# Kernel tuning notes

Hardware: AMD Instinct MI355X
Metric: run time of the kernel (lower is better)

Reference implementation:

```python
import jax, jax.numpy as jnp
import numpy as np

EMBED_DIM = 1024
N_HEADS = 16
DK = EMBED_DIM // N_HEADS


def setup_inputs() -> dict:
    key = jax.random.key(0)
    ks = jax.random.split(key, 9)
    s = 1.0 / np.sqrt(EMBED_DIM)
    d = EMBED_DIM
    return {
        "x": jax.random.normal(ks[0], (2, 2048, d), dtype=jnp.float32),
        "Wq": jax.random.uniform(ks[1], (d, d), jnp.float32, -s, s),
        "bq": jax.random.uniform(ks[2], (d,), jnp.float32, -s, s),
        "Wk": jax.random.uniform(ks[3], (d, d), jnp.float32, -s, s),
        "bk": jax.random.uniform(ks[4], (d,), jnp.float32, -s, s),
        "Wv": jax.random.uniform(ks[5], (d, d), jnp.float32, -s, s),
        "bv": jax.random.uniform(ks[6], (d,), jnp.float32, -s, s),
        "Wo": jax.random.uniform(ks[7], (d, d), jnp.float32, -s, s),
        "bo": jax.random.uniform(ks[8], (d,), jnp.float32, -s, s),
    }


def reference(x, Wq, bq, Wk, bk, Wv, bv, Wo, bo):
    B, S, D = x.shape
    H, dk = N_HEADS, DK
    # QKV projections
    q = (x @ Wq + bq).reshape(B, S, H, dk).transpose(0, 2, 1, 3)  # [B,H,S,dk]
    k = (x @ Wk + bk).reshape(B, S, H, dk).transpose(0, 2, 1, 3)
    v = (x @ Wv + bv).reshape(B, S, H, dk).transpose(0, 2, 1, 3)
    # scaled dot-product attention with full score matrix (faithful to source)
    scores = jnp.einsum("bhqd,bhkd->bhqk", q, k) / jnp.sqrt(jnp.float32(dk))
    attn = jax.nn.softmax(scores, axis=-1)
    out = jnp.einsum("bhqk,bhkd->bhqd", attn, v)  # [B,H,S,dk]
    out = out.transpose(0, 2, 1, 3).reshape(B, S, D)
    return out @ Wo + bo
```

## Files before the change

### kernel.cpp

```cpp
#include <hip/hip_runtime.h>

typedef unsigned short u16;
typedef unsigned int u32;
typedef __attribute__((ext_vector_type(8))) short short8;
typedef __attribute__((ext_vector_type(4))) float float4v;

struct alignas(8) U16x4 { u16 x, y, z, w; };

__device__ __forceinline__ u16 f2b(float f) {
    union { float f; unsigned int u; } v; v.f = f;
    unsigned int r = (v.u >> 16) & 1u;
    v.u += 0x7fffu + r;
    return (u16)(v.u >> 16);
}

__device__ __forceinline__ float b2f(u16 u) {
    union { unsigned int u; float f; } v; v.u = ((u32)u) << 16; return v.f;
}

__device__ __forceinline__ void gld16(const u16* g, u16* l) {
    __builtin_amdgcn_global_load_lds(
        (const __attribute__((address_space(1))) void*)g,
        (__attribute__((address_space(3))) void*)l, 16, 0, 0);
}

__device__ __forceinline__ short8 frag8(const u16* base, int row, int cg) {
    return *(const short8*)(base + row * 64 + ((cg ^ (row & 7)) << 3));
}

__global__ __launch_bounds__(256) void prep_kernel(
    const float* __restrict__ x, const float* __restrict__ W0,
    const float* __restrict__ W1, const float* __restrict__ W2,
    const float* __restrict__ W3, u16* __restrict__ xb,
    u16* __restrict__ T0, u16* __restrict__ T1,
    u16* __restrict__ T2, u16* __restrict__ T3) {
    __shared__ float tile[32][33];
    int id = blockIdx.x;
    if (id < 4096) {
        size_t i = ((size_t)id * 256 + threadIdx.x) * 4;
        float4 v = *(const float4*)(x + i);
        U16x4 o;
        o.x = f2b(v.x); o.y = f2b(v.y); o.z = f2b(v.z); o.w = f2b(v.w);
        *(U16x4*)(xb + i) = o;
        return;
    }
    int r = id - 4096;
    int z = r >> 10, tl = r & 1023;
    const float* W = (z == 0) ? W0 : (z == 1) ? W1 : (z == 2) ? W2 : W3;
    u16* T = (z == 0) ? T0 : (z == 1) ? T1 : (z == 2) ? T2 : T3;
    int t = threadIdx.x;
    int tx = t & 31, ty = t >> 5;
    int bn = (tl & 31) * 32, bk = (tl >> 5) * 32;
#pragma unroll
    for (int p = 0; p < 4; ++p) {
        int k = ty + p * 8;
        tile[k][tx] = W[(size_t)(bk + k) * 1024 + bn + tx];
    }
    __syncthreads();
#pragma unroll
    for (int p = 0; p < 4; ++p) {
        int n = ty + p * 8;
        T[(size_t)(bn + n) * 1024 + bk + tx] = f2b(tile[tx][n]);
    }
}

__device__ __forceinline__ void gemm_core_gld(const u16* __restrict__ A,
                                              const u16* __restrict__ BT,
                                              int m0, int n0, int t,
                                              u16* As, u16* Bs,
                                              float4v acc[4][4]) {
    int lane = t & 63, wid = t >> 6;
    int wr = wid >> 1, wc = wid & 1;
    int l16 = lane & 15, quad = lane >> 4;
    int rl = lane >> 3, cs = lane & 7;

    for (int k0 = 0; k0 < 1024; k0 += 64) {
        __syncthreads();
#pragma unroll
        for (int p = 0; p < 4; ++p) {
            int blk = wid * 4 + p;
            int row = blk * 8 + rl;
            int c = cs ^ (row & 7);
            gld16(A + (size_t)(m0 + row) * 1024 + k0 + c * 8, As + blk * 512);
            gld16(BT + (size_t)(n0 + row) * 1024 + k0 + c * 8, Bs + blk * 512);
        }
        __syncthreads();
#pragma unroll
        for (int ks = 0; ks < 64; ks += 32) {
            int cg = (ks >> 3) + quad;
            short8 af[4], bf[4];
#pragma unroll
            for (int i = 0; i < 4; ++i) af[i] = frag8(As, wr * 64 + i * 16 + l16, cg);
#pragma unroll
            for (int j = 0; j < 4; ++j) bf[j] = frag8(Bs, wc * 64 + j * 16 + l16, cg);
#pragma unroll
            for (int i = 0; i < 4; ++i)
#pragma unroll
                for (int j = 0; j < 4; ++j)
                    acc[i][j] = __builtin_amdgcn_mfma_f32_16x16x32_bf16(
                        af[i], bf[j], acc[i][j], 0, 0, 0);
        }
    }
}

__global__ __launch_bounds__(256) void qkv_kernel(
    const u16* __restrict__ X,
    const u16* __restrict__ WqT, const u16* __restrict__ WkT, const u16* __restrict__ WvT,
    const float* __restrict__ bq, const float* __restrict__ bk, const float* __restrict__ bv,
    u16* __restrict__ Qo, u16* __restrict__ Ko, u16* __restrict__ VTo) {
    __shared__ __align__(16) u16 As[128 * 64];
    __shared__ __align__(16) u16 Bs[128 * 64];
    int id = blockIdx.x;
    int m = (id & 7) | (((id >> 3) & 3) << 3);
    int nz = id >> 5;
    int n = nz & 7, z = nz >> 3;
    const u16* BT = (z == 0) ? WqT : (z == 1) ? WkT : WvT;
    const float* bias = (z == 0) ? bq : (z == 1) ? bk : bv;
    int t = threadIdx.x;
    int m0 = m * 128, n0 = n * 128;

    float4v acc[4][4];
    float4v zero4 = {0.f, 0.f, 0.f, 0.f};
#pragma unroll
    for (int i = 0; i < 4; ++i)
#pragma unroll
        for (int j = 0; j < 4; ++j) acc[i][j] = zero4;

    gemm_core_gld(X, BT, m0, n0, t, As, Bs, acc);

    int lane = t & 63, wid = t >> 6;
    int wr = wid >> 1, wc = wid & 1;
    int l16 = lane & 15, quad = lane >> 4;
    float scale = (z == 0) ? 0.18033688011112042f : 1.0f;

#pragma unroll
    for (int j = 0; j < 4; ++j) {
        int n1 = n0 + wc * 64 + j * 16 + l16;
        float bvl = bias[n1];
#pragma unroll
        for (int i = 0; i < 4; ++i) {
            int mbase = m0 + wr * 64 + i * 16 + quad * 4;
            if (z < 2) {
                u16* out = (z == 0) ? Qo : Ko;
#pragma unroll
                for (int r = 0; r < 4; ++r)
                    out[(size_t)(mbase + r) * 1024 + n1] =
                        f2b((acc[i][j][r] + bvl) * scale);
            } else {
                int bidx = mbase >> 11, s = mbase & 2047;
                size_t base =
                    ((size_t)((bidx * 16 + (n1 >> 6)) * 64 + (n1 & 63))) * 2048 + s;
                U16x4 pk;
                pk.x = f2b(acc[i][j][0] + bvl);
                pk.y = f2b(acc[i][j][1] + bvl);
                pk.z = f2b(acc[i][j][2] + bvl);
                pk.w = f2b(acc[i][j][3] + bvl);
                *(U16x4*)(VTo + base) = pk;
            }
        }
    }
}

__global__ __launch_bounds__(256) void oproj_kernel(const u16* __restrict__ X,
                                                    const u16* __restrict__ WoT,
                                                    const float* __restrict__ bias,
                                                    float* __restrict__ out) {
    __shared__ __align__(16) u16 As[128 * 64];
    __shared__ __align__(16) u16 Bs[128 * 64];
    int id = blockIdx.x;
    int m = (id & 7) | (((id >> 3) & 3) << 3);
    int n = id >> 5;
    int t = threadIdx.x;
    int m0 = m * 128, n0 = n * 128;

    float4v acc[4][4];
    float4v zero4 = {0.f, 0.f, 0.f, 0.f};
#pragma unroll
    for (int i = 0; i < 4; ++i)
#pragma unroll
        for (int j = 0; j < 4; ++j) acc[i][j] = zero4;

    gemm_core_gld(X, WoT, m0, n0, t, As, Bs, acc);

    int lane = t & 63, wid = t >> 6;
    int wr = wid >> 1, wc = wid & 1;
    int l16 = lane & 15, quad = lane >> 4;

#pragma unroll
    for (int j = 0; j < 4; ++j) {
        int n1 = n0 + wc * 64 + j * 16 + l16;
        float bvl = bias[n1];
#pragma unroll
        for (int i = 0; i < 4; ++i) {
            int mbase = m0 + wr * 64 + i * 16 + quad * 4;
#pragma unroll
            for (int r = 0; r < 4; ++r)
                out[(size_t)(mbase + r) * 1024 + n1] = acc[i][j][r] + bvl;
        }
    }
}

__global__ __launch_bounds__(128, 2) void flash_kernel(const u16* __restrict__ Q,
                                                       const u16* __restrict__ Kn,
                                                       const u16* __restrict__ VT,
                                                       u16* __restrict__ Opart,
                                                       float* __restrict__ lpart) {
    __shared__ __align__(16) u16 Ks[64 * 64];
    __shared__ __align__(16) u16 Vs[64 * 64];
    __shared__ __align__(16) u16 Ps[128][72];

    int id = blockIdx.x;
    int bh = (id & 7) | (((id >> 3) & 3) << 3);
    int rest = id >> 5;
    int qb = rest & 15, kvz = rest >> 4;
    int b = bh >> 4, h = bh & 15;
    int t = threadIdx.x;
    int wid = t >> 6, lane = t & 63;
    int l16 = lane & 15, quad = lane >> 4;
    int rl = lane >> 3, cs = lane & 7;
    int q0 = qb * 128 + wid * 64;
    size_t kbase = (size_t)(b * 2048) * 1024 + h * 64;
    size_t vbase = (size_t)(bh * 64) * 2048;

    short8 qf[4][2];
#pragma unroll
    for (int j = 0; j < 4; ++j)
#pragma unroll
        for (int kk = 0; kk < 2; ++kk)
            qf[j][kk] = *(const short8*)(
                Q + ((size_t)(b * 2048 + q0 + j * 16 + l16)) * 1024 + h * 64 +
                kk * 32 + quad * 8);

    float4v oacc[4][4], lacc[4];
    float4v zero4 = {0.f, 0.f, 0.f, 0.f};
#pragma unroll
    for (int ip = 0; ip < 4; ++ip) {
        lacc[ip] = zero4;
#pragma unroll
        for (int jd = 0; jd < 4; ++jd) oacc[ip][jd] = zero4;
    }

    const short ONE = (short)0x3F80;
    short8 ones = {ONE, ONE, ONE, ONE, ONE, ONE, ONE, ONE};

    for (int kvi = 0; kvi < 16; ++kvi) {
        int kv = kvz * 1024 + kvi * 64;
        __syncthreads();
        if (wid == 0) {
#pragma unroll
            for (int p = 0; p < 8; ++p) {
                int row = p * 8 + rl;
                int c = cs ^ (row & 7);
                gld16(Kn + kbase + (size_t)(kv + row) * 1024 + c * 8, Ks + p * 512);
            }
        } else {
#pragma unroll
            for (int p = 0; p < 8; ++p) {
                int row = p * 8 + rl;
                int c = cs ^ (row & 7);
                gld16(VT + vbase + (size_t)row * 2048 + kv + c * 8, Vs + p * 512);
            }
        }
        __syncthreads();

#pragma unroll
        for (int i = 0; i < 4; ++i) {
            float4v sacc[4];
#pragma unroll
            for (int j = 0; j < 4; ++j) sacc[j] = zero4;
#pragma unroll
            for (int kk = 0; kk < 2; ++kk) {
                short8 kf = frag8(Ks, i * 16 + l16, kk * 4 + quad);
#pragma unroll
                for (int j = 0; j < 4; ++j)
                    sacc[j] = __builtin_amdgcn_mfma_f32_16x16x32_bf16(
                        kf, qf[j][kk], sacc[j], 0, 0, 0);
            }
#pragma unroll
            for (int j = 0; j < 4; ++j) {
                u32 e0 = __float_as_uint(__builtin_amdgcn_exp2f(sacc[j][0])) + 0x8000u;
                u32 e1 = __float_as_uint(__builtin_amdgcn_exp2f(sacc[j][1])) + 0x8000u;
                u32 e2 = __float_as_uint(__builtin_amdgcn_exp2f(sacc[j][2])) + 0x8000u;
                u32 e3 = __float_as_uint(__builtin_amdgcn_exp2f(sacc[j][3])) + 0x8000u;
                uint2 pk;
                pk.x = __builtin_amdgcn_perm(e1, e0, 0x07060302u);
                pk.y = __builtin_amdgcn_perm(e3, e2, 0x07060302u);
                *(uint2*)(&Ps[wid * 64 + j * 16 + l16][i * 16 + quad * 4]) = pk;
            }
        }

#pragma unroll
        for (int kk = 0; kk < 2; ++kk) {
            int cg = kk * 4 + quad;
            short8 pf[4];
#pragma unroll
            for (int ip = 0; ip < 4; ++ip)
                pf[ip] = *(const short8*)(
                    &Ps[wid * 64 + ip * 16 + l16][kk * 32 + quad * 8]);
#pragma unroll
            for (int jd = 0; jd < 4; ++jd) {
                short8 vf = frag8(Vs, jd * 16 + l16, cg);
#pragma unroll
                for (int ip = 0; ip < 4; ++ip)
                    oacc[ip][jd] = __builtin_amdgcn_mfma_f32_16x16x32_bf16(
                        pf[ip], vf, oacc[ip][jd], 0, 0, 0);
            }
#pragma unroll
            for (int ip = 0; ip < 4; ++ip)
                lacc[ip] = __builtin_amdgcn_mfma_f32_16x16x32_bf16(
                    pf[ip], ones, lacc[ip], 0, 0, 0);
        }
    }

    size_t obase = (size_t)kvz * 4194304;
#pragma unroll
    for (int ip = 0; ip < 4; ++ip)
#pragma unroll
        for (int r = 0; r < 4; ++r) {
            int q = q0 + ip * 16 + quad * 4 + r;
#pragma unroll
            for (int jd = 0; jd < 4; ++jd)
                Opart[obase + ((size_t)(b * 2048 + q)) * 1024 + h * 64 +
                      jd * 16 + l16] = f2b(oacc[ip][jd][r]);
        }
    if (l16 == 0) {
#pragma unroll
        for (int ip = 0; ip < 4; ++ip)
#pragma unroll
            for (int r = 0; r < 4; ++r) {
                int q = q0 + ip * 16 + quad * 4 + r;
                lpart[kvz * 65536 + (b * 2048 + q) * 16 + h] = lacc[ip][r];
            }
    }
}

__global__ __launch_bounds__(256) void combine_kernel(const u16* __restrict__ Op,
                                                      const float* __restrict__ lp,
                                                      u16* __restrict__ out) {
    int idx = blockIdx.x * 256 + threadIdx.x;
    size_t i = (size_t)idx * 4;
    int qg = idx >> 8;
    int d = (idx & 255) * 4;
    int h = d >> 6;
    float l0 = lp[qg * 16 + h], l1 = lp[65536 + qg * 16 + h];
    float inv = 1.0f / (l0 + l1);
    U16x4 o0 = *(const U16x4*)(Op + i);
    U16x4 o1 = *(const U16x4*)(Op + 4194304 + i);
    U16x4 o;
    o.x = f2b((b2f(o0.x) + b2f(o1.x)) * inv);
    o.y = f2b((b2f(o0.y) + b2f(o1.y)) * inv);
    o.z = f2b((b2f(o0.z) + b2f(o1.z)) * inv);
    o.w = f2b((b2f(o0.w) + b2f(o1.w)) * inv);
    *(U16x4*)(out + i) = o;
}

extern "C" void kernel_launch(void* const* d_in, const int* in_sizes, int n_in,
                              void* d_out, int out_size, void* d_ws, size_t ws_size,
                              hipStream_t stream) {
    const float* x  = (const float*)d_in[0];
    const float* Wq = (const float*)d_in[1];
    const float* bq = (const float*)d_in[2];
    const float* Wk = (const float*)d_in[3];
    const float* bk = (const float*)d_in[4];
    const float* Wv = (const float*)d_in[5];
    const float* bv = (const float*)d_in[6];
    const float* Wo = (const float*)d_in[7];
    const float* bo = (const float*)d_in[8];
    float* out = (float*)d_out;

    char* ws = (char*)d_ws;
    const size_t MB = 1024 * 1024;
    u16* xb  = (u16*)(ws);
    u16* wqt = (u16*)(ws + 8 * MB);
    u16* wkt = (u16*)(ws + 10 * MB);
    u16* wvt = (u16*)(ws + 12 * MB);
    u16* wot = (u16*)(ws + 14 * MB);
    u16* qb_ = (u16*)(ws + 16 * MB);
    u16* kb_ = (u16*)(ws + 24 * MB);
    u16* vt_ = (u16*)(ws + 32 * MB);
    u16* ab_ = (u16*)(ws + 40 * MB);
    u16* op_ = (u16*)(ws + 48 * MB);
    float* lp_ = (float*)(ws + 64 * MB);

    prep_kernel<<<8192, 256, 0, stream>>>(x, Wq, Wk, Wv, Wo, xb,
                                          wqt, wkt, wvt, wot);
    qkv_kernel<<<768, 256, 0, stream>>>(xb, wqt, wkt, wvt, bq, bk, bv,
                                        qb_, kb_, vt_);
    flash_kernel<<<1024, 128, 0, stream>>>(qb_, kb_, vt_, op_, lp_);
    combine_kernel<<<4096, 256, 0, stream>>>(op_, lp_, ab_);
    oproj_kernel<<<256, 256, 0, stream>>>(ab_, wot, bo, out);
}
```

Baseline: 204.8 us.

## Register-prefetch K/V tiles in flash kernel and widen oproj to 8 waves

In the flash attention kernel, the direct global-to-LDS loads are replaced by register prefetching. The next K/V tile is loaded into registers while the current tile is computed, then written to LDS at the start of the next iteration. This hides global load latency at the cost of extra VGPRs, which may lower occupancy under launch_bounds(128,2). Separately, the output projection GEMM now runs 512 threads per block with an inline 8-wave tiling, each wave computing a 64x32 sub-tile, to add more waves per block for latency hiding.

```diff
diff --git a/kernel.cpp b/kernel.cpp
--- a/kernel.cpp
+++ b/kernel.cpp
@@ -161,7 +161,7 @@
     }
 }
 
-__global__ __launch_bounds__(256) void oproj_kernel(const u16* __restrict__ X,
+__global__ __launch_bounds__(512) void oproj_kernel(const u16* __restrict__ X,
                                                     const u16* __restrict__ WoT,
                                                     const float* __restrict__ bias,
                                                     float* __restrict__ out) {
@@ -172,23 +172,49 @@
     int n = id >> 5;
     int t = threadIdx.x;
     int m0 = m * 128, n0 = n * 128;
-
-    float4v acc[4][4];
+    int lane = t & 63, wid = t >> 6;
+    int wr = wid >> 2, wc = wid & 3;
+    int l16 = lane & 15, quad = lane >> 4;
+    int rl = lane >> 3, cs = lane & 7;
+
+    float4v acc[4][2];
     float4v zero4 = {0.f, 0.f, 0.f, 0.f};
 #pragma unroll
     for (int i = 0; i < 4; ++i)
 #pragma unroll
-        for (int j = 0; j < 4; ++j) acc[i][j] = zero4;
-
-    gemm_core_gld(X, WoT, m0, n0, t, As, Bs, acc);
-
-    int lane = t & 63, wid = t >> 6;
-    int wr = wid >> 1, wc = wid & 1;
-    int l16 = lane & 15, quad = lane >> 4;
-
-#pragma unroll
-    for (int j = 0; j < 4; ++j) {
-        int n1 = n0 + wc * 64 + j * 16 + l16;
+        for (int j = 0; j < 2; ++j) acc[i][j] = zero4;
+
+    for (int k0 = 0; k0 < 1024; k0 += 64) {
+        __syncthreads();
+#pragma unroll
+        for (int p = 0; p < 2; ++p) {
+            int blk = wid * 2 + p;
+            int row = blk * 8 + rl;
+            int c = cs ^ (row & 7);
+            gld16(X + (size_t)(m0 + row) * 1024 + k0 + c * 8, As + blk * 512);
+            gld16(WoT + (size_t)(n0 + row) * 1024 + k0 + c * 8, Bs + blk * 512);
+        }
+        __syncthreads();
+#pragma unroll
+        for (int ks = 0; ks < 64; ks += 32) {
+            int cg = (ks >> 3) + quad;
+            short8 af[4], bf[2];
+#pragma unroll
+            for (int i = 0; i < 4; ++i) af[i] = frag8(As, wr * 64 + i * 16 + l16, cg);
+#pragma unroll
+            for (int j = 0; j < 2; ++j) bf[j] = frag8(Bs, wc * 32 + j * 16 + l16, cg);
+#pragma unroll
+            for (int i = 0; i < 4; ++i)
+#pragma unroll
+                for (int j = 0; j < 2; ++j)
+                    acc[i][j] = __builtin_amdgcn_mfma_f32_16x16x32_bf16(
+                        af[i], bf[j], acc[i][j], 0, 0, 0);
+        }
+    }
+
+#pragma unroll
+    for (int j = 0; j < 2; ++j) {
+        int n1 = n0 + wc * 32 + j * 16 + l16;
         float bvl = bias[n1];
 #pragma unroll
         for (int i = 0; i < 4; ++i) {
@@ -221,6 +247,7 @@
     int q0 = qb * 128 + wid * 64;
     size_t kbase = (size_t)(b * 2048) * 1024 + h * 64;
     size_t vbase = (size_t)(bh * 64) * 2048;
+    u16* tile = wid ? Vs : Ks;
 
     short8 qf[4][2];
 #pragma unroll
@@ -243,25 +270,35 @@
     const short ONE = (short)0x3F80;
     short8 ones = {ONE, ONE, ONE, ONE, ONE, ONE, ONE, ONE};
 
+    int4 pref[8];
+    int kv = kvz * 1024;
+#pragma unroll
+    for (int p = 0; p < 8; ++p) {
+        int row = p * 8 + rl;
+        int c = cs ^ (row & 7);
+        pref[p] = (wid == 0)
+            ? *(const int4*)(Kn + kbase + (size_t)(kv + row) * 1024 + c * 8)
+            : *(const int4*)(VT + vbase + (size_t)row * 2048 + kv + c * 8);
+    }
+
     for (int kvi = 0; kvi < 16; ++kvi) {
-        int kv = kvz * 1024 + kvi * 64;
-        __syncthreads();
-        if (wid == 0) {
+        __syncthreads();
+#pragma unroll
+        for (int p = 0; p < 8; ++p)
+            *(int4*)(tile + p * 512 + lane * 8) = pref[p];
+        __syncthreads();
+
+        if (kvi < 15) {
+            int kvn = kv + 64;
 #pragma unroll
             for (int p = 0; p < 8; ++p) {
                 int row = p * 8 + rl;
                 int c = cs ^ (row & 7);
-                gld16(Kn + kbase + (size_t)(kv + row) * 1024 + c * 8, Ks + p * 512);
-            }
-        } else {
-#pragma unroll
-            for (int p = 0; p < 8; ++p) {
-                int row = p * 8 + rl;
-                int c = cs ^ (row & 7);
-                gld16(VT + vbase + (size_t)row * 2048 + kv + c * 8, Vs + p * 512);
-            }
-        }
-        __syncthreads();
+                pref[p] = (wid == 0)
+                    ? *(const int4*)(Kn + kbase + (size_t)(kvn + row) * 1024 + c * 8)
+                    : *(const int4*)(VT + vbase + (size_t)row * 2048 + kvn + c * 8);
+            }
+        }
 
 #pragma unroll
         for (int i = 0; i < 4; ++i) {
@@ -310,6 +347,7 @@
                 lacc[ip] = __builtin_amdgcn_mfma_f32_16x16x32_bf16(
                     pf[ip], ones, lacc[ip], 0, 0, 0);
         }
+        kv += 64;
     }
 
     size_t obase = (size_t)kvz * 4194304;
@@ -388,5 +426,5 @@
                                         qb_, kb_, vt_);
     flash_kernel<<<1024, 128, 0, stream>>>(qb_, kb_, vt_, op_, lp_);
     combine_kernel<<<4096, 256, 0, stream>>>(op_, lp_, ab_);
-    oproj_kernel<<<256, 256, 0, stream>>>(ab_, wot, bo, out);
-}
+    oproj_kernel<<<256, 512, 0, stream>>>(ab_, wot, bo, out);
+}
```

Result: slower. 254.0 us (+24.0%).
